# Performance work log

Hardware: AMD Instinct MI355X
Metric: run time of the kernel (lower is better)

## Reference

```python
import jax, jax.numpy as jnp
import numpy as np

D_MODEL = 512
TEMP = 30.0  # softmax temperature used by TransformerTrack-style RelationUnit
EPS = 1e-5
NORM_SCALE = float(np.sqrt(1.0 / (D_MODEL * 4 * 4)))


def _instance_l2norm(x):
    # x: [n, hw, b, d]; InstanceL2Norm over (dim, h, w) per (image, batch) sample
    n, hw, b, d = x.shape
    ss = jnp.sum(x * x, axis=(1, 3), keepdims=True)  # [n,1,b,1]
    return x * (NORM_SCALE * jnp.sqrt((d * hw) / (ss + EPS)))


def _cnorm(r, i):
    # joint L2 normalization of a complex vector along last axis
    s = jnp.sqrt(jnp.sum(r * r + i * i, axis=-1, keepdims=True) + 1e-12)
    return r / s, i / s


def _rel_self_attn(xr, xi, er, ei, WK):
    # xr/xi: [n, L, b, d]; er/ei: [n, L, L, b, dk] relative (helix) embeddings
    qr, qi = _cnorm(xr @ WK, xi @ WK)           # [n,L,b,dk]
    # real part of complex conjugate inner product <q, k>
    scores = (jnp.einsum('nqbk,nlbk->nbql', qr, qr)
              + jnp.einsum('nqbk,nlbk->nbql', qi, qi)
              + jnp.einsum('nqbk,nqlbk->nbql', qr, er)
              + jnp.einsum('nqbk,nqlbk->nbql', qi, ei))
    A = jax.nn.softmax(scores * TEMP, axis=-1)  # [n,b,q,l]
    out_r = jnp.einsum('nbql,nlbd->nqbd', A, xr)
    out_i = jnp.einsum('nbql,nlbd->nqbd', A, xi)
    return out_r, out_i


def _cross_attn(qr_in, qi_in, kr_in, ki_in, vr, vi, WK):
    # q: [Lq,b,d]; k,v: [Lk,b,d]
    qr, qi = _cnorm(qr_in @ WK, qi_in @ WK)
    kr, ki = _cnorm(kr_in @ WK, ki_in @ WK)
    scores = jnp.einsum('qbk,lbk->bql', qr, kr) + jnp.einsum('qbk,lbk->bql', qi, ki)
    A = jax.nn.softmax(scores * TEMP, axis=-1)
    out_r = jnp.einsum('bql,lbd->qbd', A, vr)
    out_i = jnp.einsum('bql,lbd->qbd', A, vi)
    return out_r, out_i


def _forward(src_real, src_imag, tgt_real, tgt_imag,
             src_emb_real, src_emb_imag, tgt_emb_real, tgt_emb_imag,
             pos_real, pos_imag, WK_rel, WK_cross):
    n, b, d, h, w = src_real.shape
    hw = h * w

    def tok(x):  # [n,b,d,h,w] -> [n,hw,b,d]
        return x.reshape(n, b, d, hw).transpose(0, 3, 1, 2)

    def emb(x):  # [n,b,dk,hw,hw] -> [n,hw,hw,b,dk]
        return x.transpose(0, 3, 4, 1, 2)

    sr, si = tok(src_real), tok(src_imag)
    tr, ti = tok(tgt_real), tok(tgt_imag)
    esr, esi = emb(src_emb_real), emb(src_emb_imag)
    etr, eti = emb(tgt_emb_real), emb(tgt_emb_imag)

    # ---- encoder (num_layers = 1) ----
    s2r, s2i = _rel_self_attn(sr, si, esr, esi, WK_rel)
    mem_r = _instance_l2norm(sr + s2r).reshape(n * hw, b, d)
    mem_i = _instance_l2norm(si + s2i).reshape(n * hw, b, d)

    # pos: [n,b,h,w] -> [n*hw, b, d] (broadcast over dim as in .repeat(1,1,dim))
    pr = jnp.broadcast_to(pos_real.reshape(n, b, hw).transpose(0, 2, 1).reshape(n * hw, b, 1), (n * hw, b, d))
    pi = jnp.broadcast_to(pos_imag.reshape(n, b, hw).transpose(0, 2, 1).reshape(n * hw, b, 1), (n * hw, b, d))

    def IN3(x):
        return _instance_l2norm(x.reshape(n, hw, b, d)).reshape(n * hw, b, d)

    # ---- decoder (num_layers = 1) ----
    t2r, t2i = _rel_self_attn(tr, ti, etr, eti, WK_rel)
    xr = _instance_l2norm(tr + t2r).reshape(n * hw, b, d)
    xi = _instance_l2norm(ti + t2i).reshape(n * hw, b, d)

    mask_r, mask_i = _cross_attn(xr, xi, mem_r, mem_i, pr, pi, WK_cross)
    y2r = IN3(xr * mask_r)
    y2i = IN3(xi * mask_i)

    t3r, t3i = _cross_attn(xr, xi, mem_r, mem_i, mem_r * pr, mem_i * pi, WK_cross)
    y4r = IN3(xr + t3r)
    y4i = IN3(xi + t3i)

    out_r = IN3(y2r + y4r)
    out_i = IN3(y2i + y4i)

    feat_r = out_r.reshape(n, h, w, b, d).transpose(0, 3, 4, 1, 2).reshape(n * b, d, h, w)
    feat_i = out_i.reshape(n, h, w, b, d).transpose(0, 3, 4, 1, 2).reshape(n * b, d, h, w)
    return out_r, out_i, feat_r, feat_i


def setup_inputs() -> dict:
    key = jax.random.key(0)
    ks = jax.random.split(key, 12)
    n, b, d, h, dk = 2, 2, 512, 16, 64
    hw = h * h
    inp = {
        'src_real': jax.random.normal(ks[0], (n, b, d, h, h), jnp.float32),
        'src_imag': jax.random.normal(ks[1], (n, b, d, h, h), jnp.float32),
        'tgt_real': jax.random.normal(ks[2], (n, b, d, h, h), jnp.float32),
        'tgt_imag': jax.random.normal(ks[3], (n, b, d, h, h), jnp.float32),
        'src_emb_real': jax.random.normal(ks[4], (n, b, dk, hw, hw), jnp.float32),
        'src_emb_imag': jax.random.normal(ks[5], (n, b, dk, hw, hw), jnp.float32),
        'tgt_emb_real': jax.random.normal(ks[6], (n, b, dk, hw, hw), jnp.float32),
        'tgt_emb_imag': jax.random.normal(ks[7], (n, b, dk, hw, hw), jnp.float32),
        'pos_real': jax.random.uniform(ks[8], (n, b, h, h), jnp.float32),
        'pos_imag': jax.random.uniform(ks[9], (n, b, h, h), jnp.float32),
        'WK_rel': jax.random.normal(ks[10], (d, dk), jnp.float32) * 0.02,
        'WK_cross': jax.random.normal(ks[11], (d, 128), jnp.float32) * 0.02,
    }
    return inp


def reference(src_real, src_imag, tgt_real, tgt_imag,
              src_emb_real, src_emb_imag, tgt_emb_real, tgt_emb_imag,
              pos_real, pos_imag, WK_rel, WK_cross):
    return _forward(src_real, src_imag, tgt_real, tgt_imag,
                    src_emb_real, src_emb_imag, tgt_emb_real, tgt_emb_imag,
                    pos_real, pos_imag, WK_rel, WK_cross)
```

## Files before the change

kernel.cpp:

```cpp
#include <hip/hip_runtime.h>
#include <cstdint>
#include <cstddef>

#define N_ 2
#define B_ 2
#define D_ 512
#define HW_ 256
#define DK_ 64
#define DKC_ 128
#define G_ 4
#define NBLK_ 32

constexpr size_t OFF_TSR = 0;
constexpr size_t OFF_TSI = 524288;
constexpr size_t OFF_TTR = 1048576;
constexpr size_t OFF_TTI = 1572864;
constexpr size_t OFF_QSR = 2097152;
constexpr size_t OFF_QSI = OFF_QSR + 65536;
constexpr size_t OFF_QTR = OFF_QSI + 65536;
constexpr size_t OFF_QTI = OFF_QTR + 65536;
constexpr size_t OFF_AS  = OFF_QTI + 65536;
constexpr size_t OFF_AT  = OFF_AS + 262144;
constexpr size_t OFF_YSR = OFF_AT + 262144;
constexpr size_t OFF_YSI = OFF_YSR + 524288;
constexpr size_t OFF_YTR = OFF_YSI + 524288;
constexpr size_t OFF_YTI = OFF_YTR + 524288;
constexpr size_t OFF_QCR = OFF_YTI + 524288;
constexpr size_t OFF_QCI = OFF_QCR + 131072;
constexpr size_t OFF_KCR = OFF_QCI + 131072;
constexpr size_t OFF_KCI = OFF_KCR + 131072;
constexpr size_t OFF_AC  = OFF_KCI + 131072;
constexpr size_t OFF_T3R = OFF_AC + 524288;
constexpr size_t OFF_T3I = OFF_T3R + 524288;
constexpr size_t OFF_MR  = OFF_T3I + 524288;
constexpr size_t OFF_MI  = OFF_MR + 1024;
constexpr size_t OFF_P1  = OFF_MI + 1024;
constexpr size_t OFF_P2  = OFF_P1 + 512;
constexpr size_t OFF_P3  = OFF_P2 + 512;
constexpr size_t OFF_S1  = OFF_P3 + 256;
constexpr size_t OFF_S2  = OFF_S1 + 16;
constexpr size_t OFF_SZ  = OFF_S2 + 16;

template<int NT>
__device__ __forceinline__ float blk_sum(float v, float* sh) {
  int tid = threadIdx.x;
  sh[tid] = v; __syncthreads();
  #pragma unroll
  for (int s = NT/2; s > 0; s >>= 1) { if (tid < s) sh[tid] += sh[tid+s]; __syncthreads(); }
  float r = sh[0]; __syncthreads(); return r;
}
template<int NT>
__device__ __forceinline__ float blk_max(float v, float* sh) {
  int tid = threadIdx.x;
  sh[tid] = v; __syncthreads();
  #pragma unroll
  for (int s = NT/2; s > 0; s >>= 1) { if (tid < s) sh[tid] = fmaxf(sh[tid], sh[tid+s]); __syncthreads(); }
  float r = sh[0]; __syncthreads(); return r;
}
__device__ __forceinline__ float wave_sum32(float v) {
  #pragma unroll
  for (int o = 16; o; o >>= 1) v += __shfl_xor(v, o, 64);
  return v;
}

__global__ void k_transpose(const float* sR, const float* sI, const float* tR, const float* tI, float* ws) {
  int which = blockIdx.y;
  const float* in = (which==0)? sR : (which==1)? sI : (which==2)? tR : tI;
  float* out = ws + ((which==0)? OFF_TSR : (which==1)? OFF_TSI : (which==2)? OFF_TTR : OFF_TTI);
  int bx = blockIdx.x;
  int pt = bx & 3, dt = (bx>>2)&7, nb = bx>>5;
  int ni = nb>>1, bi = nb&1;
  __shared__ float tile[64][65];
  int tid = threadIdx.x;
  int p0 = pt*64, d0 = dt*64;
  #pragma unroll
  for (int it=0; it<16; ++it) {
    int i = it*256 + tid; int row = i>>6, col = i&63;
    tile[row][col] = in[(size_t)(nb*D_ + d0+row)*HW_ + p0+col];
  }
  __syncthreads();
  #pragma unroll
  for (int it=0; it<16; ++it) {
    int i = it*256 + tid; int row = i>>6, col = i&63;
    out[(size_t)((ni*HW_ + p0+row)*B_ + bi)*D_ + d0+col] = tile[col][row];
  }
}

__global__ void __launch_bounds__(256) k_qrel(float* ws, const float* WK) {
  int bx = blockIdx.x;
  int rg = bx & 127, which = bx >> 7;
  const float* Tr = ws + (which ? OFF_TTR : OFF_TSR);
  const float* Ti = ws + (which ? OFF_TTI : OFF_TSI);
  float* Qr = ws + (which ? OFF_QTR : OFF_QSR);
  float* Qi = ws + (which ? OFF_QTI : OFF_QSI);
  int R0 = rg*8;
  __shared__ float Xr[8][512], Xi[8][512];
  int tid = threadIdx.x;
  const float4* tr4 = (const float4*)(Tr + (size_t)R0*D_);
  const float4* ti4 = (const float4*)(Ti + (size_t)R0*D_);
  #pragma unroll
  for (int it=0; it<4; ++it) {
    int i = it*256 + tid;
    ((float4*)&Xr[0][0])[i] = tr4[i];
    ((float4*)&Xi[0][0])[i] = ti4[i];
  }
  __syncthreads();
  int row = tid >> 5, col2 = (tid & 31)*2;
  float a0r=0.f, a0i=0.f, a1r=0.f, a1i=0.f;
  #pragma unroll 4
  for (int d=0; d<512; ++d) {
    float2 w = *(const float2*)&WK[(size_t)d*DK_ + col2];
    float xr = Xr[row][d], xi = Xi[row][d];
    a0r += xr*w.x; a1r += xr*w.y;
    a0i += xi*w.x; a1i += xi*w.y;
  }
  float ss = wave_sum32(a0r*a0r + a1r*a1r + a0i*a0i + a1i*a1i);
  float inv = 1.f / sqrtf(ss + 1e-12f);
  size_t o = (size_t)(R0+row)*DK_ + col2;
  Qr[o]   = a0r*inv; Qr[o+1] = a1r*inv;
  Qi[o]   = a0i*inv; Qi[o+1] = a1i*inv;
}

__global__ void __launch_bounds__(128) k_gram(float* ws) {
  int bx = blockIdx.x;
  int lt = bx & 3, qt = (bx>>2)&7, nb = (bx>>5)&3, which = bx>>7;
  int ni = nb>>1, bi = nb&1;
  const float* Qr = ws + (which ? OFF_QTR : OFF_QSR);
  const float* Qi = ws + (which ? OFF_QTI : OFF_QSI);
  float* A = ws + (which ? OFF_AT : OFF_AS) + (size_t)nb*65536;
  __shared__ float Qrs[32][33], Qis[32][33], Krs[32][68], Kis[32][68];
  int tid = threadIdx.x, ty = tid>>4, tx = tid&15;
  int ty4 = ty*4, tx4 = tx*4;
  float acc[4][4] = {};
  for (int c = 0; c < 2; ++c) {
    #pragma unroll
    for (int it = 0; it < 8; ++it) {
      int i = it*128 + tid; int row = i>>5, col = i&31;
      size_t qa = (size_t)((ni*HW_ + qt*32+row)*B_ + bi)*DK_ + c*32 + col;
      Qrs[row][col] = Qr[qa];
      Qis[row][col] = Qi[qa];
    }
    #pragma unroll
    for (int it = 0; it < 16; ++it) {
      int i = it*128 + tid; int kk = i&31, col = i>>5;
      size_t ka = (size_t)((ni*HW_ + lt*64+col)*B_ + bi)*DK_ + c*32 + kk;
      Krs[kk][col] = Qr[ka];
      Kis[kk][col] = Qi[ka];
    }
    __syncthreads();
    #pragma unroll
    for (int kk = 0; kk < 32; ++kk) {
      float4 kr = *(const float4*)&Krs[kk][tx4];
      float4 ki = *(const float4*)&Kis[kk][tx4];
      #pragma unroll
      for (int i = 0; i < 4; ++i) {
        float qr = Qrs[ty4+i][kk], qi = Qis[ty4+i][kk];
        acc[i][0] += qr*kr.x + qi*ki.x;
        acc[i][1] += qr*kr.y + qi*ki.y;
        acc[i][2] += qr*kr.z + qi*ki.z;
        acc[i][3] += qr*kr.w + qi*ki.w;
      }
    }
    __syncthreads();
  }
  #pragma unroll
  for (int i = 0; i < 4; ++i)
    #pragma unroll
    for (int j = 0; j < 4; ++j)
      A[(size_t)(qt*32+ty4+i)*256 + lt*64+tx4+j] = acc[i][j];
}

__global__ void __launch_bounds__(256, 2) k_selfattn(float* ws, const float* esr, const float* esi,
                                                     const float* etr, const float* eti) {
  int idx = blockIdx.x;
  int iq = idx & 255, nb = (idx>>8)&3, which = idx>>10;
  int ni = nb>>1, bi = nb&1;
  const float* Qr = ws + (which ? OFF_QTR : OFF_QSR);
  const float* Qi = ws + (which ? OFF_QTI : OFF_QSI);
  const float* er = which ? etr : esr;
  const float* ei = which ? eti : esi;
  float* Arow = ws + (which ? OFF_AT : OFF_AS) + (size_t)nb*65536 + (size_t)iq*256;
  __shared__ float qqr[64], qqi[64];
  int tid = threadIdx.x, w = tid>>6, lane = tid&63;
  int tokq = ni*HW_ + iq;
  if (tid < 64)       qqr[tid]    = Qr[(size_t)(tokq*B_ + bi)*DK_ + tid];
  else if (tid < 128) qqi[tid-64] = Qi[(size_t)(tokq*B_ + bi)*DK_ + (tid-64)];
  __syncthreads();
  float fr[16], fi[16];
  #pragma unroll
  for (int kk = 0; kk < 16; ++kk) { fr[kk] = qqr[w*16+kk]; fi[kk] = qqi[w*16+kk]; }
  int l0 = lane*4;
  size_t eb = (size_t)nb*4194304 + (size_t)(w*16)*65536 + (size_t)iq*256 + l0;
  const float4* er4 = (const float4*)&er[eb];
  const float4* ei4 = (const float4*)&ei[eb];
  float4 R[16], I[16];
  #pragma unroll
  for (int t = 0; t < 16; ++t) R[t] = er4[(size_t)t*16384];
  #pragma unroll
  for (int t = 0; t < 16; ++t) I[t] = ei4[(size_t)t*16384];
  float a0=0.f, a1=0.f, a2=0.f, a3=0.f;
  #pragma unroll
  for (int t = 0; t < 16; ++t) {
    a0 += fr[t]*R[t].x + fi[t]*I[t].x;
    a1 += fr[t]*R[t].y + fi[t]*I[t].y;
    a2 += fr[t]*R[t].z + fi[t]*I[t].z;
    a3 += fr[t]*R[t].w + fi[t]*I[t].w;
  }
  __shared__ float part[4][256];
  __shared__ float sh[256];
  *(float4*)&part[w][l0] = make_float4(a0,a1,a2,a3);
  __syncthreads();
  float s = (part[0][tid]+part[1][tid]+part[2][tid]+part[3][tid] + Arow[tid]) * 30.f;
  float m = blk_max<256>(s, sh);
  float e = __expf(s - m);
  float sum = blk_sum<256>(e, sh);
  Arow[tid] = e / sum;
}

__global__ void __launch_bounds__(128) k_selfapply(float* ws) {
  int bx = blockIdx.x;
  int dt = bx & 7, qt = (bx>>3)&7, nb = (bx>>6)&3, which = bx>>8;
  int ni = nb>>1, bi = nb&1;
  const float* A  = ws + (which ? OFF_AT : OFF_AS) + (size_t)nb*65536;
  const float* Xr = ws + (which ? OFF_TTR : OFF_TSR);
  const float* Xi = ws + (which ? OFF_TTI : OFF_TSI);
  float* Yr = ws + (which ? OFF_YTR : OFF_YSR);
  float* Yi = ws + (which ? OFF_YTI : OFF_YSI);
  __shared__ float As[32][33], Xrs[32][68], Xis[32][68];
  int tid = threadIdx.x, ty = tid>>4, tx = tid&15;
  int ty4 = ty*4, tx4 = tx*4;
  float ar[4][4] = {}, ai[4][4] = {};
  for (int c = 0; c < 8; ++c) {
    #pragma unroll
    for (int it = 0; it < 8; ++it) {
      int i = it*128 + tid; int row = i>>5, col = i&31;
      As[row][col] = A[(size_t)(qt*32+row)*256 + c*32+col];
    }
    #pragma unroll
    for (int it = 0; it < 16; ++it) {
      int i = it*128 + tid; int row = i>>6, col = i&63;
      size_t xb = (size_t)((ni*HW_ + c*32+row)*B_ + bi)*D_ + dt*64+col;
      Xrs[row][col] = Xr[xb]; Xis[row][col] = Xi[xb];
    }
    __syncthreads();
    #pragma unroll
    for (int kk = 0; kk < 32; ++kk) {
      float4 vr = *(const float4*)&Xrs[kk][tx4];
      float4 vi = *(const float4*)&Xis[kk][tx4];
      #pragma unroll
      for (int i = 0; i < 4; ++i) {
        float a = As[ty4+i][kk];
        ar[i][0] += a*vr.x; ar[i][1] += a*vr.y; ar[i][2] += a*vr.z; ar[i][3] += a*vr.w;
        ai[i][0] += a*vi.x; ai[i][1] += a*vi.y; ai[i][2] += a*vi.z; ai[i][3] += a*vi.w;
      }
    }
    __syncthreads();
  }
  #pragma unroll
  for (int i = 0; i < 4; ++i) {
    size_t o = (size_t)((ni*HW_ + qt*32 + ty4+i)*B_ + bi)*D_ + dt*64 + tx4;
    #pragma unroll
    for (int j = 0; j < 4; ++j) { Yr[o+j] = Xr[o+j] + ar[i][j]; Yi[o+j] = Xi[o+j] + ai[i][j]; }
  }
}

__global__ void k_reduce4(float* ws) {
  int qy = blockIdx.y;
  const float* a = ws + ((qy==0)? OFF_YSR : (qy==1)? OFF_YSI : (qy==2)? OFF_YTR : OFF_YTI);
  int g = blockIdx.x / NBLK_, blk = blockIdx.x % NBLK_;
  int ni = g>>1, bi = g&1;
  int tid = threadIdx.x;
  float acc = 0.f;
  for (int p = blk; p < HW_; p += NBLK_) {
    const float* row = a + (size_t)((ni*HW_ + p)*B_ + bi)*D_;
    for (int d = tid; d < D_; d += 256) { float v = row[d]; acc += v*v; }
  }
  __shared__ float sh[256];
  float s = blk_sum<256>(acc, sh);
  if (!tid) ws[OFF_P1 + (size_t)(qy*G_ + g)*NBLK_ + blk] = s;
}

__global__ void k_finalize(const float* part, float* scales, int nq) {
  int t = threadIdx.x;
  if (t < nq) {
    float ss = 0.f;
    for (int j = 0; j < NBLK_; ++j) ss += part[t*NBLK_ + j];
    scales[t] = 4.f * rsqrtf(ss + 1e-5f);
  }
}

__global__ void k_applyscale(float* ws, const float* scales) {
  int qy = blockIdx.y;
  float* a = ws + ((qy==0)? OFF_YSR : (qy==1)? OFF_YSI : (qy==2)? OFF_YTR : OFF_YTI);
  int idx4 = blockIdx.x*256 + threadIdx.x;
  int elem = idx4*4;
  int bi = (elem / D_) & 1;
  int r = elem >> 10;
  int ni = r >> 8;
  float s = scales[qy*G_ + ni*2 + bi];
  float4 v = ((float4*)a)[idx4];
  v.x *= s; v.y *= s; v.z *= s; v.w *= s;
  ((float4*)a)[idx4] = v;
}

__global__ void __launch_bounds__(256) k_crossproj(float* ws, const float* W) {
  int bx = blockIdx.x;
  int rg = bx & 127, isK = bx >> 7;
  const float* inR = ws + (isK ? OFF_YSR : OFF_YTR);
  const float* inI = ws + (isK ? OFF_YSI : OFF_YTI);
  float* oR = ws + (isK ? OFF_KCR : OFF_QCR);
  float* oI = ws + (isK ? OFF_KCI : OFF_QCI);
  int R0 = rg*8;
  __shared__ float Xr[8][512], Xi[8][512];
  int tid = threadIdx.x;
  const float4* xr4 = (const float4*)(inR + (size_t)R0*D_);
  const float4* xi4 = (const float4*)(inI + (size_t)R0*D_);
  #pragma unroll
  for (int it=0; it<4; ++it) {
    int i = it*256 + tid;
    ((float4*)&Xr[0][0])[i] = xr4[i];
    ((float4*)&Xi[0][0])[i] = xi4[i];
  }
  __syncthreads();
  int row = tid >> 5, col4 = (tid & 31)*4;
  float ar[4]={}, ai[4]={};
  #pragma unroll 4
  for (int d=0; d<512; ++d) {
    float4 w = *(const float4*)&W[(size_t)d*DKC_ + col4];
    float xr = Xr[row][d], xi = Xi[row][d];
    ar[0] += xr*w.x; ar[1] += xr*w.y; ar[2] += xr*w.z; ar[3] += xr*w.w;
    ai[0] += xi*w.x; ai[1] += xi*w.y; ai[2] += xi*w.z; ai[3] += xi*w.w;
  }
  float ps = ar[0]*ar[0]+ar[1]*ar[1]+ar[2]*ar[2]+ar[3]*ar[3]
           + ai[0]*ai[0]+ai[1]*ai[1]+ai[2]*ai[2]+ai[3]*ai[3];
  float ss = wave_sum32(ps);
  float inv = 1.f / sqrtf(ss + 1e-12f);
  size_t o = (size_t)(R0+row)*DKC_ + col4;
  oR[o]   = ar[0]*inv; oR[o+1] = ar[1]*inv; oR[o+2] = ar[2]*inv; oR[o+3] = ar[3]*inv;
  oI[o]   = ai[0]*inv; oI[o+1] = ai[1]*inv; oI[o+2] = ai[2]*inv; oI[o+3] = ai[3]*inv;
}

__global__ void __launch_bounds__(128) k_crossscore(float* ws) {
  int bx = blockIdx.x;
  int lt = bx & 7, qt = (bx>>3)&15, bi = bx>>7;
  const float* Qr = ws + OFF_QCR; const float* Qi = ws + OFF_QCI;
  const float* Kr = ws + OFF_KCR; const float* Ki = ws + OFF_KCI;
  float* S = ws + OFF_AC + (size_t)bi*262144;
  __shared__ float Qrs[32][33], Qis[32][33], Krs[32][68], Kis[32][68];
  int tid = threadIdx.x, ty = tid>>4, tx = tid&15;
  int ty4 = ty*4, tx4 = tx*4;
  float acc[4][4] = {};
  for (int c = 0; c < 4; ++c) {
    #pragma unroll
    for (int it = 0; it < 8; ++it) {
      int i = it*128 + tid; int row = i>>5, col = i&31;
      Qrs[row][col] = Qr[(size_t)((qt*32+row)*B_ + bi)*DKC_ + c*32 + col];
      Qis[row][col] = Qi[(size_t)((qt*32+row)*B_ + bi)*DKC_ + c*32 + col];
    }
    #pragma unroll
    for (int it = 0; it < 16; ++it) {
      int i = it*128 + tid; int kk = i&31, col = i>>5;
      Krs[kk][col] = Kr[(size_t)((lt*64+col)*B_ + bi)*DKC_ + c*32 + kk];
      Kis[kk][col] = Ki[(size_t)((lt*64+col)*B_ + bi)*DKC_ + c*32 + kk];
    }
    __syncthreads();
    #pragma unroll
    for (int kk = 0; kk < 32; ++kk) {
      float4 kr = *(const float4*)&Krs[kk][tx4];
      float4 ki = *(const float4*)&Kis[kk][tx4];
      #pragma unroll
      for (int i = 0; i < 4; ++i) {
        float qr = Qrs[ty4+i][kk], qi = Qis[ty4+i][kk];
        acc[i][0] += qr*kr.x + qi*ki.x;
        acc[i][1] += qr*kr.y + qi*ki.y;
        acc[i][2] += qr*kr.z + qi*ki.z;
        acc[i][3] += qr*kr.w + qi*ki.w;
      }
    }
    __syncthreads();
  }
  #pragma unroll
  for (int i = 0; i < 4; ++i)
    #pragma unroll
    for (int j = 0; j < 4; ++j)
      S[(size_t)(qt*32+ty4+i)*512 + lt*64+tx4+j] = acc[i][j];
}

__global__ void k_softmaxrow(float* ws, const float* posr, const float* posi) {
  int bx = blockIdx.x;
  int bi = bx >> 9, iq = bx & 511;
  float* row = ws + OFF_AC + (size_t)bi*262144 + (size_t)iq*512;
  int tid = threadIdx.x;
  float s0 = row[tid]*30.f, s1 = row[tid+256]*30.f;
  __shared__ float sh[256];
  float m = blk_max<256>(fmaxf(s0, s1), sh);
  float e0 = __expf(s0 - m), e1 = __expf(s1 - m);
  float sum = blk_sum<256>(e0 + e1, sh);
  float inv = 1.f / sum;
  float a0 = e0*inv, a1 = e1*inv;
  row[tid] = a0; row[tid+256] = a1;
  float pr0 = posr[bi*HW_ + tid],        pr1 = posr[(B_+bi)*HW_ + tid];
  float pi0 = posi[bi*HW_ + tid],        pi1 = posi[(B_+bi)*HW_ + tid];
  float mr = blk_sum<256>(a0*pr0 + a1*pr1, sh);
  float mi = blk_sum<256>(a0*pi0 + a1*pi1, sh);
  if (!tid) { ws[OFF_MR + bi*512 + iq] = mr; ws[OFF_MI + bi*512 + iq] = mi; }
}

__global__ void __launch_bounds__(128) k_crossapply(float* ws, const float* posr, const float* posi) {
  int bx = blockIdx.x;
  int dt = bx & 7, qt = (bx>>3)&15, bi = (bx>>7)&1, kc = bx>>8;
  const float* A  = ws + OFF_AC + (size_t)bi*262144;
  const float* Mr = ws + OFF_YSR; const float* Mi = ws + OFF_YSI;
  float* Pr = ws + (kc ? OFF_TSR : OFF_T3R);
  float* Pi = ws + (kc ? OFF_TSI : OFF_T3I);
  __shared__ float As[32][33], Vrs[32][68], Vis[32][68];
  int tid = threadIdx.x, ty = tid>>4, tx = tid&15;
  int ty4 = ty*4, tx4 = tx*4;
  float ar[4][4] = {}, ai[4][4] = {};
  for (int c = 0; c < 8; ++c) {
    int kb = kc*256 + c*32;
    #pragma unroll
    for (int it = 0; it < 8; ++it) {
      int i = it*128 + tid; int row = i>>5, col = i&31;
      As[row][col] = A[(size_t)(qt*32+row)*512 + kb+col];
    }
    #pragma unroll
    for (int it = 0; it < 16; ++it) {
      int i = it*128 + tid; int row = i>>6, col = i&63;
      int l = kb + row; int nil = l>>8, pl = l&255;
      float pvr = posr[(nil*B_ + bi)*HW_ + pl];
      float pvi = posi[(nil*B_ + bi)*HW_ + pl];
      size_t vb = (size_t)(l*B_ + bi)*D_ + dt*64+col;
      Vrs[row][col] = Mr[vb] * pvr;
      Vis[row][col] = Mi[vb] * pvi;
    }
    __syncthreads();
    #pragma unroll
    for (int kk = 0; kk < 32; ++kk) {
      float4 vr = *(const float4*)&Vrs[kk][tx4];
      float4 vi = *(const float4*)&Vis[kk][tx4];
      #pragma unroll
      for (int i = 0; i < 4; ++i) {
        float a = As[ty4+i][kk];
        ar[i][0] += a*vr.x; ar[i][1] += a*vr.y; ar[i][2] += a*vr.z; ar[i][3] += a*vr.w;
        ai[i][0] += a*vi.x; ai[i][1] += a*vi.y; ai[i][2] += a*vi.z; ai[i][3] += a*vi.w;
      }
    }
    __syncthreads();
  }
  #pragma unroll
  for (int i = 0; i < 4; ++i) {
    size_t o = (size_t)((qt*32+ty4+i)*B_ + bi)*D_ + dt*64 + tx4;
    #pragma unroll
    for (int j = 0; j < 4; ++j) { Pr[o+j] = ar[i][j]; Pi[o+j] = ai[i][j]; }
  }
}

__global__ void k_reducey24(float* ws) {
  int qy = blockIdx.y;
  int g = blockIdx.x / NBLK_, blk = blockIdx.x % NBLK_;
  int ni = g>>1, bi = g&1;
  const float* X   = ws + ((qy==0 || qy==2) ? OFF_YTR : OFF_YTI);
  const float* T3a = ws + ((qy==2) ? OFF_T3R : OFF_T3I);
  const float* T3b = ws + ((qy==2) ? OFF_TSR : OFF_TSI);
  const float* M   = ws + ((qy==0) ? OFF_MR : OFF_MI);
  int tid = threadIdx.x;
  float acc = 0.f;
  for (int p = blk; p < HW_; p += NBLK_) {
    int l = ni*HW_ + p;
    size_t rb = (size_t)(l*B_ + bi)*D_;
    if (qy < 2) {
      float m = M[bi*512 + l];
      for (int d = tid; d < D_; d += 256) { float v = X[rb+d]*m; acc += v*v; }
    } else {
      for (int d = tid; d < D_; d += 256) { float v = X[rb+d] + T3a[rb+d] + T3b[rb+d]; acc += v*v; }
    }
  }
  __shared__ float sh[256];
  float s = blk_sum<256>(acc, sh);
  if (!tid) ws[OFF_P2 + (size_t)(qy*G_ + g)*NBLK_ + blk] = s;
}

__global__ void k_combine(float* ws, const float* scales2) {
  int y = blockIdx.y;
  int g = blockIdx.x / NBLK_, blk = blockIdx.x % NBLK_;
  int ni = g>>1, bi = g&1;
  const float* X   = ws + (y ? OFF_YTI : OFF_YTR);
  float* T3a       = ws + (y ? OFF_T3I : OFF_T3R);
  const float* T3b = ws + (y ? OFF_TSI : OFF_TSR);
  const float* M   = ws + (y ? OFF_MI : OFF_MR);
  float a2 = scales2[y*G_ + g], a4 = scales2[(2+y)*G_ + g];
  int tid = threadIdx.x;
  float acc = 0.f;
  for (int p = blk; p < HW_; p += NBLK_) {
    int l = ni*HW_ + p;
    float m = M[bi*512 + l];
    size_t rb = (size_t)(l*B_ + bi)*D_;
    for (int d = tid; d < D_; d += 256) {
      float x = X[rb+d];
      float z = a2*(x*m) + a4*(x + T3a[rb+d] + T3b[rb+d]);
      T3a[rb+d] = z;
      acc += z*z;
    }
  }
  __shared__ float sh[256];
  float s = blk_sum<256>(acc, sh);
  if (!tid) ws[OFF_P3 + (size_t)(y*G_ + g)*NBLK_ + blk] = s;
}

__global__ void k_final(float* ws, const float* scalesZ, float* out) {
  int y = blockIdx.y;
  int bx = blockIdx.x;
  int pt = bx & 3, dt = (bx>>2)&7, nb = bx>>5;
  int ni = nb>>1, bi = nb&1;
  const float* Z = ws + (y ? OFF_T3I : OFF_T3R);
  float s = scalesZ[y*G_ + nb];
  float* o1 = out + (size_t)y*524288;
  float* o2 = out + (size_t)(2+y)*524288;
  __shared__ float tile[64][65];
  int tid = threadIdx.x;
  int p0 = pt*64, d0 = dt*64;
  #pragma unroll
  for (int it = 0; it < 16; ++it) {
    int i = it*256 + tid; int row = i>>6, col = i&63;
    size_t idx = (size_t)((ni*HW_ + p0+row)*B_ + bi)*D_ + d0+col;
    float v = Z[idx] * s;
    o1[idx] = v;
    tile[row][col] = v;
  }
  __syncthreads();
  #pragma unroll
  for (int it = 0; it < 16; ++it) {
    int i = it*256 + tid; int row = i>>6, col = i&63;
    o2[(size_t)(nb*D_ + d0+row)*HW_ + p0+col] = tile[col][row];
  }
}

extern "C" void kernel_launch(void* const* d_in, const int* in_sizes, int n_in,
                              void* d_out, int out_size, void* d_ws, size_t ws_size,
                              hipStream_t stream) {
  const float* srcR = (const float*)d_in[0];
  const float* srcI = (const float*)d_in[1];
  const float* tgtR = (const float*)d_in[2];
  const float* tgtI = (const float*)d_in[3];
  const float* esr  = (const float*)d_in[4];
  const float* esi  = (const float*)d_in[5];
  const float* etr  = (const float*)d_in[6];
  const float* eti  = (const float*)d_in[7];
  const float* posR = (const float*)d_in[8];
  const float* posI = (const float*)d_in[9];
  const float* WKrel   = (const float*)d_in[10];
  const float* WKcross = (const float*)d_in[11];
  float* ws  = (float*)d_ws;
  float* out = (float*)d_out;

  k_transpose <<<dim3(128,4), 256, 0, stream>>>(srcR, srcI, tgtR, tgtI, ws);
  k_qrel      <<<256, 256, 0, stream>>>(ws, WKrel);
  k_gram      <<<256, 128, 0, stream>>>(ws);
  k_selfattn  <<<2048, 256, 0, stream>>>(ws, esr, esi, etr, eti);
  k_selfapply <<<512, 128, 0, stream>>>(ws);
  k_reduce4   <<<dim3(G_*NBLK_,4), 256, 0, stream>>>(ws);
  k_finalize  <<<1, 64, 0, stream>>>(ws + OFF_P1, ws + OFF_S1, 16);
  k_applyscale<<<dim3(512,4), 256, 0, stream>>>(ws, ws + OFF_S1);
  k_crossproj <<<256, 256, 0, stream>>>(ws, WKcross);
  k_crossscore<<<256, 128, 0, stream>>>(ws);
  k_softmaxrow<<<1024, 256, 0, stream>>>(ws, posR, posI);
  k_crossapply<<<512, 128, 0, stream>>>(ws, posR, posI);
  k_reducey24 <<<dim3(G_*NBLK_,4), 256, 0, stream>>>(ws);
  k_finalize  <<<1, 64, 0, stream>>>(ws + OFF_P2, ws + OFF_S2, 16);
  k_combine   <<<dim3(G_*NBLK_,2), 256, 0, stream>>>(ws, ws + OFF_S2);
  k_finalize  <<<1, 64, 0, stream>>>(ws + OFF_P3, ws + OFF_SZ, 8);
  k_final     <<<dim3(128,2), 256, 0, stream>>>(ws, ws + OFF_SZ, out);
}
```

Before: 290.2 us.

## Map one wave per query row in relative self-attention with double-buffered loads

The self-attention score kernel now assigns each wavefront a whole query row over all 64 dk channels, so it no longer splits dk across four waves and sums partials through shared memory. The softmax max and sum become wave shuffles instead of block-wide shared-memory reductions, and the query vector is broadcast with shuffles. Embedding loads are issued in 8-channel chunks into two register buffers, with sched barriers so loads overlap the FMAs. The grid shrinks to a quarter as many blocks, which lowers the number of blocks in flight and relies on the load pipelining to hide the memory latency of this bandwidth-bound read of the embeddings.

```diff
diff --git a/kernel.cpp b/kernel.cpp
--- a/kernel.cpp
+++ b/kernel.cpp
@@ -62,6 +62,16 @@
   for (int o = 16; o; o >>= 1) v += __shfl_xor(v, o, 64);
   return v;
 }
+__device__ __forceinline__ float wave_sum64(float v) {
+  #pragma unroll
+  for (int o = 32; o; o >>= 1) v += __shfl_xor(v, o, 64);
+  return v;
+}
+__device__ __forceinline__ float wave_max64(float v) {
+  #pragma unroll
+  for (int o = 32; o; o >>= 1) v = fmaxf(v, __shfl_xor(v, o, 64));
+  return v;
+}
 
 __global__ void k_transpose(const float* sR, const float* sI, const float* tR, const float* tI, float* ws) {
   int which = blockIdx.y;
@@ -170,51 +180,69 @@
       A[(size_t)(qt*32+ty4+i)*256 + lt*64+tx4+j] = acc[i][j];
 }
 
+#define LOADCH(BR, BI, C)                                        \
+  _Pragma("unroll")                                              \
+  for (int t = 0; t < 8; ++t) {                                  \
+    BR[t] = er4[(size_t)((C)*8 + t) * 16384];                    \
+    BI[t] = ei4[(size_t)((C)*8 + t) * 16384];                    \
+  }                                                              \
+  __builtin_amdgcn_sched_barrier(0);
+#define CONSUME(BR, BI, K0)                                      \
+  _Pragma("unroll")                                              \
+  for (int t = 0; t < 8; ++t) {                                  \
+    float fr = __shfl(qvr, (K0) + t);                            \
+    float fi = __shfl(qvi, (K0) + t);                            \
+    a0 += fr*BR[t].x + fi*BI[t].x;                               \
+    a1 += fr*BR[t].y + fi*BI[t].y;                               \
+    a2 += fr*BR[t].z + fi*BI[t].z;                               \
+    a3 += fr*BR[t].w + fi*BI[t].w;                               \
+  }                                                              \
+  __builtin_amdgcn_sched_barrier(0);
+
 __global__ void __launch_bounds__(256, 2) k_selfattn(float* ws, const float* esr, const float* esi,
                                                      const float* etr, const float* eti) {
   int idx = blockIdx.x;
-  int iq = idx & 255, nb = (idx>>8)&3, which = idx>>10;
+  int qg = idx & 63, nb = (idx>>6)&3, which = idx>>8;
   int ni = nb>>1, bi = nb&1;
   const float* Qr = ws + (which ? OFF_QTR : OFF_QSR);
   const float* Qi = ws + (which ? OFF_QTI : OFF_QSI);
   const float* er = which ? etr : esr;
   const float* ei = which ? eti : esi;
+  int tid = threadIdx.x, w = tid>>6, lane = tid&63;
+  int iq = qg*4 + w;
   float* Arow = ws + (which ? OFF_AT : OFF_AS) + (size_t)nb*65536 + (size_t)iq*256;
-  __shared__ float qqr[64], qqi[64];
-  int tid = threadIdx.x, w = tid>>6, lane = tid&63;
   int tokq = ni*HW_ + iq;
-  if (tid < 64)       qqr[tid]    = Qr[(size_t)(tokq*B_ + bi)*DK_ + tid];
-  else if (tid < 128) qqi[tid-64] = Qi[(size_t)(tokq*B_ + bi)*DK_ + (tid-64)];
-  __syncthreads();
-  float fr[16], fi[16];
-  #pragma unroll
-  for (int kk = 0; kk < 16; ++kk) { fr[kk] = qqr[w*16+kk]; fi[kk] = qqi[w*16+kk]; }
+  float qvr = Qr[(size_t)(tokq*B_ + bi)*DK_ + lane];
+  float qvi = Qi[(size_t)(tokq*B_ + bi)*DK_ + lane];
   int l0 = lane*4;
-  size_t eb = (size_t)nb*4194304 + (size_t)(w*16)*65536 + (size_t)iq*256 + l0;
+  size_t eb = (size_t)nb*4194304 + (size_t)iq*256 + l0;
   const float4* er4 = (const float4*)&er[eb];
   const float4* ei4 = (const float4*)&ei[eb];
-  float4 R[16], I[16];
-  #pragma unroll
-  for (int t = 0; t < 16; ++t) R[t] = er4[(size_t)t*16384];
-  #pragma unroll
-  for (int t = 0; t < 16; ++t) I[t] = ei4[(size_t)t*16384];
+  float4 Ra[8], Ia[8], Rb[8], Ib[8];
   float a0=0.f, a1=0.f, a2=0.f, a3=0.f;
-  #pragma unroll
-  for (int t = 0; t < 16; ++t) {
-    a0 += fr[t]*R[t].x + fi[t]*I[t].x;
-    a1 += fr[t]*R[t].y + fi[t]*I[t].y;
-    a2 += fr[t]*R[t].z + fi[t]*I[t].z;
-    a3 += fr[t]*R[t].w + fi[t]*I[t].w;
-  }
-  __shared__ float part[4][256];
-  __shared__ float sh[256];
-  *(float4*)&part[w][l0] = make_float4(a0,a1,a2,a3);
-  __syncthreads();
-  float s = (part[0][tid]+part[1][tid]+part[2][tid]+part[3][tid] + Arow[tid]) * 30.f;
-  float m = blk_max<256>(s, sh);
-  float e = __expf(s - m);
-  float sum = blk_sum<256>(e, sh);
-  Arow[tid] = e / sum;
+  LOADCH(Ra, Ia, 0)
+  LOADCH(Rb, Ib, 1)
+  CONSUME(Ra, Ia, 0)
+  LOADCH(Ra, Ia, 2)
+  CONSUME(Rb, Ib, 8)
+  LOADCH(Rb, Ib, 3)
+  CONSUME(Ra, Ia, 16)
+  LOADCH(Ra, Ia, 4)
+  CONSUME(Rb, Ib, 24)
+  LOADCH(Rb, Ib, 5)
+  CONSUME(Ra, Ia, 32)
+  LOADCH(Ra, Ia, 6)
+  CONSUME(Rb, Ib, 40)
+  LOADCH(Rb, Ib, 7)
+  CONSUME(Ra, Ia, 48)
+  CONSUME(Rb, Ib, 56)
+  float4 g = *(const float4*)&Arow[l0];
+  float s0 = (a0 + g.x)*30.f, s1 = (a1 + g.y)*30.f;
+  float s2 = (a2 + g.z)*30.f, s3 = (a3 + g.w)*30.f;
+  float m = wave_max64(fmaxf(fmaxf(s0,s1), fmaxf(s2,s3)));
+  float e0 = __expf(s0-m), e1 = __expf(s1-m), e2 = __expf(s2-m), e3 = __expf(s3-m);
+  float inv = 1.f / wave_sum64(e0+e1+e2+e3);
+  *(float4*)&Arow[l0] = make_float4(e0*inv, e1*inv, e2*inv, e3*inv);
 }
 
 __global__ void __launch_bounds__(128) k_selfapply(float* ws) {
@@ -557,7 +585,7 @@
   k_transpose <<<dim3(128,4), 256, 0, stream>>>(srcR, srcI, tgtR, tgtI, ws);
   k_qrel      <<<256, 256, 0, stream>>>(ws, WKrel);
   k_gram      <<<256, 128, 0, stream>>>(ws);
-  k_selfattn  <<<2048, 256, 0, stream>>>(ws, esr, esi, etr, eti);
+  k_selfattn  <<<512, 256, 0, stream>>>(ws, esr, esi, etr, eti);
   k_selfapply <<<512, 128, 0, stream>>>(ws);
   k_reduce4   <<<dim3(G_*NBLK_,4), 256, 0, stream>>>(ws);
   k_finalize  <<<1, 64, 0, stream>>>(ws + OFF_P1, ws + OFF_S1, 16);
```

New measurement: 292.5 us. No clear change (+0.8%).

## Fold instance-norm scales into consumers and pipeline self-attn embedding loads

Applied to the files above, without the earlier changes.

Removes the three single-block finalize kernels and the separate apply-scale pass. Each consumer kernel now recomputes its instance-L2 scale from the partial sums and applies it inline, so a full read-modify-write pass over four 512K-float buffers and four launches go away. The self-attention score kernel swaps its 16-deep register load of embeddings for a double-buffered, 4-chunk load/consume schedule pinned with sched_barrier. It also gets query values through wave shuffles instead of shared memory and raises launch_bounds to 4 blocks, aiming for more occupancy and load overlap. The cost is redundant per-thread scale reductions and more dependence on the compiler honouring the barriers.

```diff
diff --git a/kernel.cpp b/kernel.cpp
--- a/kernel.cpp
+++ b/kernel.cpp
@@ -37,9 +37,6 @@
 constexpr size_t OFF_P1  = OFF_MI + 1024;
 constexpr size_t OFF_P2  = OFF_P1 + 512;
 constexpr size_t OFF_P3  = OFF_P2 + 512;
-constexpr size_t OFF_S1  = OFF_P3 + 256;
-constexpr size_t OFF_S2  = OFF_S1 + 16;
-constexpr size_t OFF_SZ  = OFF_S2 + 16;
 
 template<int NT>
 __device__ __forceinline__ float blk_sum(float v, float* sh) {
@@ -61,6 +58,12 @@
   #pragma unroll
   for (int o = 16; o; o >>= 1) v += __shfl_xor(v, o, 64);
   return v;
+}
+__device__ __forceinline__ float scale_from(const float* part, int q) {
+  float ss = 0.f;
+  #pragma unroll
+  for (int j = 0; j < NBLK_; ++j) ss += part[q*NBLK_ + j];
+  return 4.f * rsqrtf(ss + 1e-5f);
 }
 
 __global__ void k_transpose(const float* sR, const float* sI, const float* tR, const float* tI, float* ws) {
@@ -170,7 +173,26 @@
       A[(size_t)(qt*32+ty4+i)*256 + lt*64+tx4+j] = acc[i][j];
 }
 
-__global__ void __launch_bounds__(256, 2) k_selfattn(float* ws, const float* esr, const float* esi,
+#define LOAD4(BR, BI, C)                                         \
+  _Pragma("unroll")                                              \
+  for (int t = 0; t < 4; ++t) {                                  \
+    BR[t] = er4[(size_t)((C)*4 + t) * 16384];                    \
+    BI[t] = ei4[(size_t)((C)*4 + t) * 16384];                    \
+  }                                                              \
+  __builtin_amdgcn_sched_barrier(0);
+#define CONS4(BR, BI, K0)                                        \
+  _Pragma("unroll")                                              \
+  for (int t = 0; t < 4; ++t) {                                  \
+    float fr = __shfl(qvr, (K0) + t);                            \
+    float fi = __shfl(qvi, (K0) + t);                            \
+    a0 += fr*BR[t].x + fi*BI[t].x;                               \
+    a1 += fr*BR[t].y + fi*BI[t].y;                               \
+    a2 += fr*BR[t].z + fi*BI[t].z;                               \
+    a3 += fr*BR[t].w + fi*BI[t].w;                               \
+  }                                                              \
+  __builtin_amdgcn_sched_barrier(0);
+
+__global__ void __launch_bounds__(256, 4) k_selfattn(float* ws, const float* esr, const float* esi,
                                                      const float* etr, const float* eti) {
   int idx = blockIdx.x;
   int iq = idx & 255, nb = (idx>>8)&3, which = idx>>10;
@@ -180,32 +202,25 @@
   const float* er = which ? etr : esr;
   const float* ei = which ? eti : esi;
   float* Arow = ws + (which ? OFF_AT : OFF_AS) + (size_t)nb*65536 + (size_t)iq*256;
-  __shared__ float qqr[64], qqi[64];
   int tid = threadIdx.x, w = tid>>6, lane = tid&63;
   int tokq = ni*HW_ + iq;
-  if (tid < 64)       qqr[tid]    = Qr[(size_t)(tokq*B_ + bi)*DK_ + tid];
-  else if (tid < 128) qqi[tid-64] = Qi[(size_t)(tokq*B_ + bi)*DK_ + (tid-64)];
-  __syncthreads();
-  float fr[16], fi[16];
-  #pragma unroll
-  for (int kk = 0; kk < 16; ++kk) { fr[kk] = qqr[w*16+kk]; fi[kk] = qqi[w*16+kk]; }
+  int kl = lane & 15;
+  float qvr = Qr[(size_t)(tokq*B_ + bi)*DK_ + w*16 + kl];
+  float qvi = Qi[(size_t)(tokq*B_ + bi)*DK_ + w*16 + kl];
   int l0 = lane*4;
   size_t eb = (size_t)nb*4194304 + (size_t)(w*16)*65536 + (size_t)iq*256 + l0;
   const float4* er4 = (const float4*)&er[eb];
   const float4* ei4 = (const float4*)&ei[eb];
-  float4 R[16], I[16];
-  #pragma unroll
-  for (int t = 0; t < 16; ++t) R[t] = er4[(size_t)t*16384];
-  #pragma unroll
-  for (int t = 0; t < 16; ++t) I[t] = ei4[(size_t)t*16384];
+  float4 Ra[4], Ia[4], Rb[4], Ib[4];
   float a0=0.f, a1=0.f, a2=0.f, a3=0.f;
-  #pragma unroll
-  for (int t = 0; t < 16; ++t) {
-    a0 += fr[t]*R[t].x + fi[t]*I[t].x;
-    a1 += fr[t]*R[t].y + fi[t]*I[t].y;
-    a2 += fr[t]*R[t].z + fi[t]*I[t].z;
-    a3 += fr[t]*R[t].w + fi[t]*I[t].w;
-  }
+  LOAD4(Ra, Ia, 0)
+  LOAD4(Rb, Ib, 1)
+  CONS4(Ra, Ia, 0)
+  LOAD4(Ra, Ia, 2)
+  CONS4(Rb, Ib, 4)
+  LOAD4(Rb, Ib, 3)
+  CONS4(Ra, Ia, 8)
+  CONS4(Rb, Ib, 12)
   __shared__ float part[4][256];
   __shared__ float sh[256];
   *(float4*)&part[w][l0] = make_float4(a0,a1,a2,a3);
@@ -280,29 +295,6 @@
   if (!tid) ws[OFF_P1 + (size_t)(qy*G_ + g)*NBLK_ + blk] = s;
 }
 
-__global__ void k_finalize(const float* part, float* scales, int nq) {
-  int t = threadIdx.x;
-  if (t < nq) {
-    float ss = 0.f;
-    for (int j = 0; j < NBLK_; ++j) ss += part[t*NBLK_ + j];
-    scales[t] = 4.f * rsqrtf(ss + 1e-5f);
-  }
-}
-
-__global__ void k_applyscale(float* ws, const float* scales) {
-  int qy = blockIdx.y;
-  float* a = ws + ((qy==0)? OFF_YSR : (qy==1)? OFF_YSI : (qy==2)? OFF_YTR : OFF_YTI);
-  int idx4 = blockIdx.x*256 + threadIdx.x;
-  int elem = idx4*4;
-  int bi = (elem / D_) & 1;
-  int r = elem >> 10;
-  int ni = r >> 8;
-  float s = scales[qy*G_ + ni*2 + bi];
-  float4 v = ((float4*)a)[idx4];
-  v.x *= s; v.y *= s; v.z *= s; v.w *= s;
-  ((float4*)a)[idx4] = v;
-}
-
 __global__ void __launch_bounds__(256) k_crossproj(float* ws, const float* W) {
   int bx = blockIdx.x;
   int rg = bx & 127, isK = bx >> 7;
@@ -331,11 +323,17 @@
     ar[0] += xr*w.x; ar[1] += xr*w.y; ar[2] += xr*w.z; ar[3] += xr*w.w;
     ai[0] += xi*w.x; ai[1] += xi*w.y; ai[2] += xi*w.z; ai[3] += xi*w.w;
   }
+  int rr = R0 + row;
+  int bi = rr & 1, gg = ((rr>>1)>>8)*2 + bi;
+  float sR = scale_from(ws + OFF_P1, (isK?0:2)*G_ + gg);
+  float sI = scale_from(ws + OFF_P1, (isK?1:3)*G_ + gg);
+  ar[0]*=sR; ar[1]*=sR; ar[2]*=sR; ar[3]*=sR;
+  ai[0]*=sI; ai[1]*=sI; ai[2]*=sI; ai[3]*=sI;
   float ps = ar[0]*ar[0]+ar[1]*ar[1]+ar[2]*ar[2]+ar[3]*ar[3]
            + ai[0]*ai[0]+ai[1]*ai[1]+ai[2]*ai[2]+ai[3]*ai[3];
   float ss = wave_sum32(ps);
   float inv = 1.f / sqrtf(ss + 1e-12f);
-  size_t o = (size_t)(R0+row)*DKC_ + col4;
+  size_t o = (size_t)rr*DKC_ + col4;
   oR[o]   = ar[0]*inv; oR[o+1] = ar[1]*inv; oR[o+2] = ar[2]*inv; oR[o+3] = ar[3]*inv;
   oI[o]   = ai[0]*inv; oI[o+1] = ai[1]*inv; oI[o+2] = ai[2]*inv; oI[o+3] = ai[3]*inv;
 }
@@ -413,6 +411,8 @@
   const float* Mr = ws + OFF_YSR; const float* Mi = ws + OFF_YSI;
   float* Pr = ws + (kc ? OFF_TSR : OFF_T3R);
   float* Pi = ws + (kc ? OFF_TSI : OFF_T3I);
+  float smr = scale_from(ws + OFF_P1, 0*G_ + kc*2 + bi);
+  float smi = scale_from(ws + OFF_P1, 1*G_ + kc*2 + bi);
   __shared__ float As[32][33], Vrs[32][68], Vis[32][68];
   int tid = threadIdx.x, ty = tid>>4, tx = tid&15;
   int ty4 = ty*4, tx4 = tx*4;
@@ -427,9 +427,9 @@
     #pragma unroll
     for (int it = 0; it < 16; ++it) {
       int i = it*128 + tid; int row = i>>6, col = i&63;
-      int l = kb + row; int nil = l>>8, pl = l&255;
-      float pvr = posr[(nil*B_ + bi)*HW_ + pl];
-      float pvi = posi[(nil*B_ + bi)*HW_ + pl];
+      int l = kb + row; int pl = l & 255;
+      float pvr = posr[(kc*B_ + bi)*HW_ + pl] * smr;
+      float pvi = posi[(kc*B_ + bi)*HW_ + pl] * smi;
       size_t vb = (size_t)(l*B_ + bi)*D_ + dt*64+col;
       Vrs[row][col] = Mr[vb] * pvr;
       Vis[row][col] = Mi[vb] * pvi;
@@ -464,16 +464,17 @@
   const float* T3a = ws + ((qy==2) ? OFF_T3R : OFF_T3I);
   const float* T3b = ws + ((qy==2) ? OFF_TSR : OFF_TSI);
   const float* M   = ws + ((qy==0) ? OFF_MR : OFF_MI);
+  float sx = scale_from(ws + OFF_P1, ((qy==0||qy==2) ? 2 : 3)*G_ + g);
   int tid = threadIdx.x;
   float acc = 0.f;
   for (int p = blk; p < HW_; p += NBLK_) {
     int l = ni*HW_ + p;
     size_t rb = (size_t)(l*B_ + bi)*D_;
     if (qy < 2) {
-      float m = M[bi*512 + l];
+      float m = M[bi*512 + l] * sx;
       for (int d = tid; d < D_; d += 256) { float v = X[rb+d]*m; acc += v*v; }
     } else {
-      for (int d = tid; d < D_; d += 256) { float v = X[rb+d] + T3a[rb+d] + T3b[rb+d]; acc += v*v; }
+      for (int d = tid; d < D_; d += 256) { float v = X[rb+d]*sx + T3a[rb+d] + T3b[rb+d]; acc += v*v; }
     }
   }
   __shared__ float sh[256];
@@ -481,7 +482,7 @@
   if (!tid) ws[OFF_P2 + (size_t)(qy*G_ + g)*NBLK_ + blk] = s;
 }
 
-__global__ void k_combine(float* ws, const float* scales2) {
+__global__ void k_combine(float* ws) {
   int y = blockIdx.y;
   int g = blockIdx.x / NBLK_, blk = blockIdx.x % NBLK_;
   int ni = g>>1, bi = g&1;
@@ -489,7 +490,9 @@
   float* T3a       = ws + (y ? OFF_T3I : OFF_T3R);
   const float* T3b = ws + (y ? OFF_TSI : OFF_TSR);
   const float* M   = ws + (y ? OFF_MI : OFF_MR);
-  float a2 = scales2[y*G_ + g], a4 = scales2[(2+y)*G_ + g];
+  float sx = scale_from(ws + OFF_P1, (2+y)*G_ + g);
+  float a2 = scale_from(ws + OFF_P2, y*G_ + g);
+  float a4 = scale_from(ws + OFF_P2, (2+y)*G_ + g);
   int tid = threadIdx.x;
   float acc = 0.f;
   for (int p = blk; p < HW_; p += NBLK_) {
@@ -497,7 +500,7 @@
     float m = M[bi*512 + l];
     size_t rb = (size_t)(l*B_ + bi)*D_;
     for (int d = tid; d < D_; d += 256) {
-      float x = X[rb+d];
+      float x = X[rb+d] * sx;
       float z = a2*(x*m) + a4*(x + T3a[rb+d] + T3b[rb+d]);
       T3a[rb+d] = z;
       acc += z*z;
@@ -508,13 +511,13 @@
   if (!tid) ws[OFF_P3 + (size_t)(y*G_ + g)*NBLK_ + blk] = s;
 }
 
-__global__ void k_final(float* ws, const float* scalesZ, float* out) {
+__global__ void k_final(float* ws, float* out) {
   int y = blockIdx.y;
   int bx = blockIdx.x;
   int pt = bx & 3, dt = (bx>>2)&7, nb = bx>>5;
   int ni = nb>>1, bi = nb&1;
   const float* Z = ws + (y ? OFF_T3I : OFF_T3R);
-  float s = scalesZ[y*G_ + nb];
+  float s = scale_from(ws + OFF_P3, y*G_ + nb);
   float* o1 = out + (size_t)y*524288;
   float* o2 = out + (size_t)(2+y)*524288;
   __shared__ float tile[64][65];
@@ -560,15 +563,11 @@
   k_selfattn  <<<2048, 256, 0, stream>>>(ws, esr, esi, etr, eti);
   k_selfapply <<<512, 128, 0, stream>>>(ws);
   k_reduce4   <<<dim3(G_*NBLK_,4), 256, 0, stream>>>(ws);
-  k_finalize  <<<1, 64, 0, stream>>>(ws + OFF_P1, ws + OFF_S1, 16);
-  k_applyscale<<<dim3(512,4), 256, 0, stream>>>(ws, ws + OFF_S1);
   k_crossproj <<<256, 256, 0, stream>>>(ws, WKcross);
   k_crossscore<<<256, 128, 0, stream>>>(ws);
   k_softmaxrow<<<1024, 256, 0, stream>>>(ws, posR, posI);
   k_crossapply<<<512, 128, 0, stream>>>(ws, posR, posI);
   k_reducey24 <<<dim3(G_*NBLK_,4), 256, 0, stream>>>(ws);
-  k_finalize  <<<1, 64, 0, stream>>>(ws + OFF_P2, ws + OFF_S2, 16);
-  k_combine   <<<dim3(G_*NBLK_,2), 256, 0, stream>>>(ws, ws + OFF_S2);
-  k_finalize  <<<1, 64, 0, stream>>>(ws + OFF_P3, ws + OFF_SZ, 8);
-  k_final     <<<dim3(128,2), 256, 0, stream>>>(ws, ws + OFF_SZ, out);
-}
+  k_combine   <<<dim3(G_*NBLK_,2), 256, 0, stream>>>(ws);
+  k_final     <<<dim3(128,2), 256, 0, stream>>>(ws, out);
+}
```

After: 283.9 us. 2.2% less time.
